# Kernel optimization log

Hardware: AMD Instinct MI355X
Metric: run time of the kernel (lower is better)

## Reference

```python
import jax, jax.numpy as jnp
from jax import lax
import numpy as np

KERNEL = 32
ORISIZE = 256
EPS = 1e-5


def _avgpool(x, k):
    # x: [B, C, H, W] -> [B, C, H-k+1, W-k+1], stride 1, VALID
    s = lax.reduce_window(x, 0.0, lax.add, (1, 1, k, k), (1, 1, 1, 1), 'VALID')
    return s / float(k * k)


def setup_inputs() -> dict:
    key = jax.random.key(0)
    k1, k2, k3, k4 = jax.random.split(key, 4)
    B, C = 32, 64
    return {
        'infeat': jax.random.normal(k1, (B, 2, ORISIZE, ORISIZE), jnp.float32),
        'labelTpesudo': jax.random.uniform(k2, (B, 1, ORISIZE, ORISIZE), jnp.float32),
        'labelT': jax.random.uniform(k3, (B, 1, ORISIZE, ORISIZE), jnp.float32),
        'FeatureDA': jax.random.normal(k4, (B, C, ORISIZE, ORISIZE), jnp.float32),
        'k': 2,
    }


def reference(infeat, labelTpesudo, labelT, FeatureDA, k):
    B = infeat.shape[0]
    P = ORISIZE - KERNEL + 1  # poolSize = 225
    half = KERNEL // 2        # suppression half-window = 16

    prob = jax.nn.softmax(infeat, axis=1)                      # F.softmax default dim=1 for 4D
    ent = -prob * jnp.log(prob + EPS)                          # Entropy()
    entP = jnp.sum(_avgpool(ent, KERNEL), axis=1)              # [B, P, P]
    featP = _avgpool(prob, KERNEL)                             # [B, 2, P, P]

    def extract(src, py, px):  # src [C,H,W] -> [C,KERNEL,KERNEL]
        return lax.dynamic_slice(src, (0, py, px), (src.shape[0], KERNEL, KERNEL))
    extract_b = jax.vmap(extract, in_axes=(0, 0, 0))

    grid = jnp.arange(P)
    cls_list, feat_list, lp_list, lt_list, val_list, oxy_list = [], [], [], [], [], []

    for c in range(2):  # class loop (unchg, chg)
        mask = jnp.ones((B, P, P), infeat.dtype)
        for _kk in range(k):  # greedy top-k with suppression
            filt = (featP[:, c] - 0.1 * entP) * mask           # [B, P, P]
            flat = filt.reshape(B, -1)
            idx = jnp.argmax(flat, axis=1)                     # topk k=1
            vals = jnp.take_along_axis(flat, idx[:, None], axis=1)[:, 0]
            py = idx // P
            px = idx % P
            # suppression box in pooled coords (half-open, clipped to [0, P])
            y0 = jnp.maximum(0, py - half); y1 = jnp.minimum(P, py + half)
            x0 = jnp.maximum(0, px - half); x1 = jnp.minimum(P, px + half)
            box = ((grid[None, :, None] >= y0[:, None, None]) & (grid[None, :, None] < y1[:, None, None]) &
                   (grid[None, None, :] >= x0[:, None, None]) & (grid[None, None, :] < x1[:, None, None]))
            mask = mask * (1.0 - box.astype(mask.dtype))
            # patch extraction in image coords: py,px <= P-1 so 32x32 always fits
            cls_list.append(extract_b(infeat, py, px))
            feat_list.append(extract_b(FeatureDA, py, px))
            lp_list.append(extract_b(labelTpesudo, py, px))
            lt_list.append(extract_b(labelT, py, px))
            val_list.append(vals)
            ox = jnp.stack([px, px + KERNEL - 1], axis=1)
            oy = jnp.stack([py, py + KERNEL - 1], axis=1)
            oxy_list.append(jnp.stack([ox, oy], axis=1).astype(jnp.int32))  # [B,2,2]

    classiferT = jnp.concatenate(cls_list, axis=0)   # [2*k*B, 2, 32, 32]
    patchFeatDA = jnp.concatenate(feat_list, axis=0)  # [2*k*B, C, 32, 32]
    labelpesudo = jnp.concatenate(lp_list, axis=0)
    labelTTrue = jnp.concatenate(lt_list, axis=0)
    provalue = jnp.concatenate(val_list, axis=0)      # [2*k*B]
    pointXY = jnp.concatenate(oxy_list, axis=0)       # [2*k*B, 2, 2]
    return classiferT, patchFeatDA, labelpesudo, labelTTrue, provalue, pointXY
```

## Files before the change

### kernel.cpp

```cpp
#include <hip/hip_runtime.h>
#include <math.h>

#define ORISIZE 256
#define KER 32
#define P 225
#define PP (P * P)
#define HALF 16
#define FEPS 1e-5f

__global__ __launch_bounds__(256) void field_hpool_kernel(
    const float* __restrict__ infeat, float* __restrict__ Hp,
    float* __restrict__ He) {
  int b = blockIdx.x >> 8;
  int y = blockIdx.x & 255;
  int x = threadIdx.x;

  __shared__ float sp[ORISIZE];
  __shared__ float se[ORISIZE];

  const float* r0 = infeat + ((size_t)(b * 2 + 0) * ORISIZE + y) * ORISIZE;
  const float* r1 = infeat + ((size_t)(b * 2 + 1) * ORISIZE + y) * ORISIZE;
  float a0 = r0[x];
  float a1 = r1[x];
  float m = fmaxf(a0, a1);
  float e0 = expf(a0 - m);
  float e1 = expf(a1 - m);
  float s = e0 + e1;
  float p0 = e0 / s;
  float p1 = e1 / s;
  float ent = -(p0 * logf(p0 + FEPS)) - (p1 * logf(p1 + FEPS));
  sp[x] = p0;
  se[x] = ent;
  __syncthreads();

  if (x < P) {
    float accp = 0.f, acce = 0.f;
#pragma unroll
    for (int dx = 0; dx < KER; ++dx) {
      accp += sp[x + dx];
      acce += se[x + dx];
    }
    size_t o = ((size_t)b * ORISIZE + y) * P + x;
    Hp[o] = accp;
    He[o] = acce;
  }
}

__global__ __launch_bounds__(256) void vpool_kernel(
    const float* __restrict__ Hp, const float* __restrict__ He,
    float* __restrict__ SP, float* __restrict__ EP, int total) {
  int idx = blockIdx.x * blockDim.x + threadIdx.x;
  if (idx >= total) return;
  int b = idx / PP;
  int r = idx - b * PP;
  int py = r / P;
  int px = r - py * P;
  const float* hp = Hp + ((size_t)b * ORISIZE + py) * P + px;
  const float* he = He + ((size_t)b * ORISIZE + py) * P + px;
  float a = 0.f, e = 0.f;
#pragma unroll
  for (int dy = 0; dy < KER; ++dy) {
    a += hp[(size_t)dy * P];
    e += he[(size_t)dy * P];
  }
  SP[idx] = a * (1.f / (KER * KER));
  EP[idx] = e * (1.f / (KER * KER));
}

__global__ __launch_bounds__(256) void select_kernel(
    const float* __restrict__ SP, const float* __restrict__ EP, int B, int K,
    float* __restrict__ out_val, float* __restrict__ out_xy,
    int* __restrict__ selyx) {
  int bc = blockIdx.x;
  int b = bc % B;
  int c = bc / B;
  int tid = threadIdx.x;

  __shared__ float rv[256];
  __shared__ int ri[256];
  __shared__ int bys[16], bxs[16];

  const float* sp = SP + (size_t)b * PP;
  const float* ep = EP + (size_t)b * PP;

  for (int kk = 0; kk < K; ++kk) {
    float best = -INFINITY;
    int bi = PP;
    for (int i = tid; i < PP; i += 256) {
      int py = i / P;
      int px = i - py * P;
      float sv = sp[i];
      float ev = ep[i];
      float v = ((c == 0) ? sv : 1.0f - sv) - 0.1f * ev;
      bool masked = false;
      for (int j = 0; j < kk; ++j) {
        if (py >= bys[j] - HALF && py < bys[j] + HALF && px >= bxs[j] - HALF &&
            px < bxs[j] + HALF)
          masked = true;
      }
      if (masked) v = 0.0f;
      if (v > best) {
        best = v;
        bi = i;
      }
    }
    rv[tid] = best;
    ri[tid] = bi;
    __syncthreads();
    for (int sh = 128; sh > 0; sh >>= 1) {
      if (tid < sh) {
        float v2 = rv[tid + sh];
        int i2 = ri[tid + sh];
        if (v2 > rv[tid] || (v2 == rv[tid] && i2 < ri[tid])) {
          rv[tid] = v2;
          ri[tid] = i2;
        }
      }
      __syncthreads();
    }
    if (tid == 0) {
      int idx = ri[0];
      int py = idx / P;
      int px = idx - py * P;
      bys[kk] = py;
      bxs[kk] = px;
      int slot = (c * K + kk) * B + b;
      out_val[slot] = rv[0];
      out_xy[slot * 4 + 0] = (float)px;
      out_xy[slot * 4 + 1] = (float)(px + KER - 1);
      out_xy[slot * 4 + 2] = (float)py;
      out_xy[slot * 4 + 3] = (float)(py + KER - 1);
      selyx[slot * 2 + 0] = py;
      selyx[slot * 2 + 1] = px;
    }
    __syncthreads();
  }
}

__global__ __launch_bounds__(256) void extract_kernel(
    const float* __restrict__ src, float* __restrict__ dst,
    const int* __restrict__ selyx, int Csrc, int B, int total) {
  int idx = blockIdx.x * blockDim.x + threadIdx.x;
  if (idx >= total) return;
  int per = Csrc * KER * KER;
  int slot = idx / per;
  int r = idx - slot * per;
  int ch = r / (KER * KER);
  int rr = r - ch * (KER * KER);
  int dy = rr >> 5;
  int dx = rr & 31;
  int b = slot % B;
  int py = selyx[slot * 2 + 0];
  int px = selyx[slot * 2 + 1];
  dst[idx] =
      src[(((size_t)b * Csrc + ch) * ORISIZE + (py + dy)) * ORISIZE + (px + dx)];
}

extern "C" void kernel_launch(void* const* d_in, const int* in_sizes, int n_in,
                              void* d_out, int out_size, void* d_ws,
                              size_t ws_size, hipStream_t stream) {
  const float* infeat = (const float*)d_in[0];
  const float* labelTpesudo = (const float*)d_in[1];
  const float* labelT = (const float*)d_in[2];
  const float* FeatureDA = (const float*)d_in[3];

  int B = in_sizes[0] / (2 * ORISIZE * ORISIZE);
  int C = in_sizes[3] / (B * ORISIZE * ORISIZE);
  long per_patch = (long)(C + 4) * KER * KER + 5;
  int K = (int)((long)out_size / (2L * B * per_patch));
  if (K < 1) K = 1;
  if (K > 16) K = 16;
  int npatch = 2 * K * B;

  float* Hp = (float*)d_ws;
  float* He = Hp + (size_t)B * ORISIZE * P;
  float* SP = He + (size_t)B * ORISIZE * P;
  float* EP = SP + (size_t)B * PP;
  int* selyx = (int*)(EP + (size_t)B * PP);

  float* out = (float*)d_out;
  size_t o_cls = 0;
  size_t o_feat = o_cls + (size_t)npatch * 2 * KER * KER;
  size_t o_lp = o_feat + (size_t)npatch * C * KER * KER;
  size_t o_lt = o_lp + (size_t)npatch * 1 * KER * KER;
  size_t o_val = o_lt + (size_t)npatch * 1 * KER * KER;
  size_t o_xy = o_val + (size_t)npatch;

  field_hpool_kernel<<<dim3(B * ORISIZE), dim3(256), 0, stream>>>(infeat, Hp,
                                                                  He);

  int totalv = B * PP;
  vpool_kernel<<<dim3((totalv + 255) / 256), dim3(256), 0, stream>>>(
      Hp, He, SP, EP, totalv);

  select_kernel<<<dim3(2 * B), dim3(256), 0, stream>>>(
      SP, EP, B, K, out + o_val, out + o_xy, selyx);

  int t_cls = npatch * 2 * KER * KER;
  extract_kernel<<<dim3((t_cls + 255) / 256), dim3(256), 0, stream>>>(
      infeat, out + o_cls, selyx, 2, B, t_cls);
  int t_feat = npatch * C * KER * KER;
  extract_kernel<<<dim3((t_feat + 255) / 256), dim3(256), 0, stream>>>(
      FeatureDA, out + o_feat, selyx, C, B, t_feat);
  int t_lab = npatch * 1 * KER * KER;
  extract_kernel<<<dim3((t_lab + 255) / 256), dim3(256), 0, stream>>>(
      labelTpesudo, out + o_lp, selyx, 1, B, t_lab);
  extract_kernel<<<dim3((t_lab + 255) / 256), dim3(256), 0, stream>>>(
      labelT, out + o_lt, selyx, 1, B, t_lab);
}
```

Before: 806.7 us.

## Split greedy argmax across many blocks per round and fuse patch extraction

The single-block-per-(batch,class) selection kernel, which ran only 64 blocks, is replaced by one launch per greedy round. Each launch spreads the pooled map over 32 blocks per (batch,class) and reduces the partial maxima in the next round or in a small finish kernel. The pooling kernel now writes the combined per-class score map directly, so selection no longer recomputes it. The four extraction launches are merged into one kernel. The cost is extra launches per round and a small re-reduction of the partial results in every block.

New measurement: 707.5 us. 12.3% less time.

```diff
diff --git a/kernel.cpp b/kernel.cpp
--- a/kernel.cpp
+++ b/kernel.cpp
@@ -7,6 +7,8 @@
 #define PP (P * P)
 #define HALF 16
 #define FEPS 1e-5f
+#define NSPLIT 32
+#define CHUNK ((PP + NSPLIT - 1) / NSPLIT)
 
 __global__ __launch_bounds__(256) void field_hpool_kernel(
     const float* __restrict__ infeat, float* __restrict__ Hp,
@@ -48,7 +50,7 @@
 
 __global__ __launch_bounds__(256) void vpool_kernel(
     const float* __restrict__ Hp, const float* __restrict__ He,
-    float* __restrict__ SP, float* __restrict__ EP, int total) {
+    float* __restrict__ F, int B, int total) {
   int idx = blockIdx.x * blockDim.x + threadIdx.x;
   if (idx >= total) return;
   int b = idx / PP;
@@ -63,97 +65,153 @@
     a += hp[(size_t)dy * P];
     e += he[(size_t)dy * P];
   }
-  SP[idx] = a * (1.f / (KER * KER));
-  EP[idx] = e * (1.f / (KER * KER));
-}
-
-__global__ __launch_bounds__(256) void select_kernel(
-    const float* __restrict__ SP, const float* __restrict__ EP, int B, int K,
+  float sv = a * (1.f / (KER * KER));
+  float ev = e * (1.f / (KER * KER));
+  F[(size_t)(0 * B + b) * PP + r] = sv - 0.1f * ev;
+  F[(size_t)(1 * B + b) * PP + r] = (1.0f - sv) - 0.1f * ev;
+}
+
+__global__ __launch_bounds__(256) void argmax_round_kernel(
+    const float* __restrict__ F, float* __restrict__ pval,
+    int* __restrict__ pidx, int B, int kk) {
+  int s = blockIdx.x;
+  int b = blockIdx.y;
+  int c = blockIdx.z;
+  int tid = threadIdx.x;
+
+  __shared__ int bys[16], bxs[16];
+  __shared__ float rv[256];
+  __shared__ int ri[256];
+
+  if (tid < kk) {
+    int j = tid;
+    int pbase = ((j * B + b) * 2 + c) * NSPLIT;
+    float bv = -INFINITY;
+    int bi = PP;
+    for (int ss = 0; ss < NSPLIT; ++ss) {
+      float v = pval[pbase + ss];
+      int ii = pidx[pbase + ss];
+      if (v > bv || (v == bv && ii < bi)) { bv = v; bi = ii; }
+    }
+    int py = bi / P;
+    bys[j] = py;
+    bxs[j] = bi - py * P;
+  }
+  __syncthreads();
+
+  const float* f = F + ((size_t)c * B + b) * PP;
+  int base = s * CHUNK;
+  int end = base + CHUNK;
+  if (end > PP) end = PP;
+
+  float best = -INFINITY;
+  int bi = PP;
+  for (int i = base + tid; i < end; i += 256) {
+    float v = f[i];
+    int py = i / P;
+    int px = i - py * P;
+    bool masked = false;
+    for (int j = 0; j < kk; ++j) {
+      if (py >= bys[j] - HALF && py < bys[j] + HALF && px >= bxs[j] - HALF &&
+          px < bxs[j] + HALF)
+        masked = true;
+    }
+    if (masked) v = 0.0f;
+    if (v > best) {
+      best = v;
+      bi = i;
+    }
+  }
+  rv[tid] = best;
+  ri[tid] = bi;
+  __syncthreads();
+  for (int sh = 128; sh > 0; sh >>= 1) {
+    if (tid < sh) {
+      float v2 = rv[tid + sh];
+      int i2 = ri[tid + sh];
+      if (v2 > rv[tid] || (v2 == rv[tid] && i2 < ri[tid])) {
+        rv[tid] = v2;
+        ri[tid] = i2;
+      }
+    }
+    __syncthreads();
+  }
+  if (tid == 0) {
+    int p = ((kk * B + b) * 2 + c) * NSPLIT + s;
+    pval[p] = rv[0];
+    pidx[p] = ri[0];
+  }
+}
+
+__global__ __launch_bounds__(256) void finish_kernel(
+    const float* __restrict__ pval, const int* __restrict__ pidx, int B, int K,
     float* __restrict__ out_val, float* __restrict__ out_xy,
     int* __restrict__ selyx) {
-  int bc = blockIdx.x;
-  int b = bc % B;
-  int c = bc / B;
-  int tid = threadIdx.x;
-
-  __shared__ float rv[256];
-  __shared__ int ri[256];
-  __shared__ int bys[16], bxs[16];
-
-  const float* sp = SP + (size_t)b * PP;
-  const float* ep = EP + (size_t)b * PP;
-
-  for (int kk = 0; kk < K; ++kk) {
-    float best = -INFINITY;
+  int total = B * 2 * K;
+  for (int t = blockIdx.x * blockDim.x + threadIdx.x; t < total;
+       t += gridDim.x * blockDim.x) {
+    int c = t & 1;
+    int rem = t >> 1;
+    int b = rem % B;
+    int kk = rem / B;
+    int pbase = ((kk * B + b) * 2 + c) * NSPLIT;
+    float bv = -INFINITY;
     int bi = PP;
-    for (int i = tid; i < PP; i += 256) {
-      int py = i / P;
-      int px = i - py * P;
-      float sv = sp[i];
-      float ev = ep[i];
-      float v = ((c == 0) ? sv : 1.0f - sv) - 0.1f * ev;
-      bool masked = false;
-      for (int j = 0; j < kk; ++j) {
-        if (py >= bys[j] - HALF && py < bys[j] + HALF && px >= bxs[j] - HALF &&
-            px < bxs[j] + HALF)
-          masked = true;
-      }
-      if (masked) v = 0.0f;
-      if (v > best) {
-        best = v;
-        bi = i;
-      }
-    }
-    rv[tid] = best;
-    ri[tid] = bi;
-    __syncthreads();
-    for (int sh = 128; sh > 0; sh >>= 1) {
-      if (tid < sh) {
-        float v2 = rv[tid + sh];
-        int i2 = ri[tid + sh];
-        if (v2 > rv[tid] || (v2 == rv[tid] && i2 < ri[tid])) {
-          rv[tid] = v2;
-          ri[tid] = i2;
-        }
-      }
-      __syncthreads();
-    }
-    if (tid == 0) {
-      int idx = ri[0];
-      int py = idx / P;
-      int px = idx - py * P;
-      bys[kk] = py;
-      bxs[kk] = px;
-      int slot = (c * K + kk) * B + b;
-      out_val[slot] = rv[0];
-      out_xy[slot * 4 + 0] = (float)px;
-      out_xy[slot * 4 + 1] = (float)(px + KER - 1);
-      out_xy[slot * 4 + 2] = (float)py;
-      out_xy[slot * 4 + 3] = (float)(py + KER - 1);
-      selyx[slot * 2 + 0] = py;
-      selyx[slot * 2 + 1] = px;
-    }
-    __syncthreads();
-  }
-}
-
-__global__ __launch_bounds__(256) void extract_kernel(
-    const float* __restrict__ src, float* __restrict__ dst,
-    const int* __restrict__ selyx, int Csrc, int B, int total) {
+    for (int ss = 0; ss < NSPLIT; ++ss) {
+      float v = pval[pbase + ss];
+      int ii = pidx[pbase + ss];
+      if (v > bv || (v == bv && ii < bi)) { bv = v; bi = ii; }
+    }
+    int py = bi / P;
+    int px = bi - py * P;
+    int slot = (c * K + kk) * B + b;
+    out_val[slot] = bv;
+    out_xy[slot * 4 + 0] = (float)px;
+    out_xy[slot * 4 + 1] = (float)(px + KER - 1);
+    out_xy[slot * 4 + 2] = (float)py;
+    out_xy[slot * 4 + 3] = (float)(py + KER - 1);
+    selyx[slot * 2 + 0] = py;
+    selyx[slot * 2 + 1] = px;
+  }
+}
+
+__global__ __launch_bounds__(256) void extract_all_kernel(
+    const float* __restrict__ infeat, const float* __restrict__ FeatureDA,
+    const float* __restrict__ lp, const float* __restrict__ lt,
+    const int* __restrict__ selyx, int B, int C, int total,
+    float* __restrict__ out, size_t o_feat, size_t o_lp, size_t o_lt) {
   int idx = blockIdx.x * blockDim.x + threadIdx.x;
   if (idx >= total) return;
-  int per = Csrc * KER * KER;
+  int TC = C + 4;
+  int per = TC * KER * KER;
   int slot = idx / per;
-  int r = idx - slot * per;
-  int ch = r / (KER * KER);
-  int rr = r - ch * (KER * KER);
-  int dy = rr >> 5;
-  int dx = rr & 31;
+  int rem = idx - slot * per;
+  int tc = rem >> 10;
+  int pix = rem & 1023;
+  int dy = pix >> 5;
+  int dx = pix & 31;
   int b = slot % B;
   int py = selyx[slot * 2 + 0];
   int px = selyx[slot * 2 + 1];
-  dst[idx] =
-      src[(((size_t)b * Csrc + ch) * ORISIZE + (py + dy)) * ORISIZE + (px + dx)];
+
+  const float* src;
+  int ch, srcC;
+  size_t dsto;
+  if (tc < 2) {
+    src = infeat; ch = tc; srcC = 2;
+    dsto = ((size_t)slot * 2 + ch) * 1024;
+  } else if (tc < 2 + C) {
+    src = FeatureDA; ch = tc - 2; srcC = C;
+    dsto = o_feat + ((size_t)slot * C + ch) * 1024;
+  } else if (tc == 2 + C) {
+    src = lp; ch = 0; srcC = 1;
+    dsto = o_lp + (size_t)slot * 1024;
+  } else {
+    src = lt; ch = 0; srcC = 1;
+    dsto = o_lt + (size_t)slot * 1024;
+  }
+  out[dsto + pix] =
+      src[(((size_t)b * srcC + ch) * ORISIZE + (py + dy)) * ORISIZE + (px + dx)];
 }
 
 extern "C" void kernel_launch(void* const* d_in, const int* in_sizes, int n_in,
@@ -174,16 +232,16 @@
 
   float* Hp = (float*)d_ws;
   float* He = Hp + (size_t)B * ORISIZE * P;
-  float* SP = He + (size_t)B * ORISIZE * P;
-  float* EP = SP + (size_t)B * PP;
-  int* selyx = (int*)(EP + (size_t)B * PP);
+  float* F = He + (size_t)B * ORISIZE * P;
+  float* pval = F + (size_t)2 * B * PP;
+  int* pidx = (int*)(pval + (size_t)16 * B * 2 * NSPLIT);
+  int* selyx = pidx + (size_t)16 * B * 2 * NSPLIT;
 
   float* out = (float*)d_out;
-  size_t o_cls = 0;
-  size_t o_feat = o_cls + (size_t)npatch * 2 * KER * KER;
+  size_t o_feat = (size_t)npatch * 2 * KER * KER;
   size_t o_lp = o_feat + (size_t)npatch * C * KER * KER;
-  size_t o_lt = o_lp + (size_t)npatch * 1 * KER * KER;
-  size_t o_val = o_lt + (size_t)npatch * 1 * KER * KER;
+  size_t o_lt = o_lp + (size_t)npatch * KER * KER;
+  size_t o_val = o_lt + (size_t)npatch * KER * KER;
   size_t o_xy = o_val + (size_t)npatch;
 
   field_hpool_kernel<<<dim3(B * ORISIZE), dim3(256), 0, stream>>>(infeat, Hp,
@@ -191,20 +249,18 @@
 
   int totalv = B * PP;
   vpool_kernel<<<dim3((totalv + 255) / 256), dim3(256), 0, stream>>>(
-      Hp, He, SP, EP, totalv);
-
-  select_kernel<<<dim3(2 * B), dim3(256), 0, stream>>>(
-      SP, EP, B, K, out + o_val, out + o_xy, selyx);
-
-  int t_cls = npatch * 2 * KER * KER;
-  extract_kernel<<<dim3((t_cls + 255) / 256), dim3(256), 0, stream>>>(
-      infeat, out + o_cls, selyx, 2, B, t_cls);
-  int t_feat = npatch * C * KER * KER;
-  extract_kernel<<<dim3((t_feat + 255) / 256), dim3(256), 0, stream>>>(
-      FeatureDA, out + o_feat, selyx, C, B, t_feat);
-  int t_lab = npatch * 1 * KER * KER;
-  extract_kernel<<<dim3((t_lab + 255) / 256), dim3(256), 0, stream>>>(
-      labelTpesudo, out + o_lp, selyx, 1, B, t_lab);
-  extract_kernel<<<dim3((t_lab + 255) / 256), dim3(256), 0, stream>>>(
-      labelT, out + o_lt, selyx, 1, B, t_lab);
-}
+      Hp, He, F, B, totalv);
+
+  for (int kk = 0; kk < K; ++kk) {
+    argmax_round_kernel<<<dim3(NSPLIT, B, 2), dim3(256), 0, stream>>>(
+        F, pval, pidx, B, kk);
+  }
+  finish_kernel<<<dim3(1), dim3(256), 0, stream>>>(pval, pidx, B, K,
+                                                   out + o_val, out + o_xy,
+                                                   selyx);
+
+  int total = npatch * (C + 4) * KER * KER;
+  extract_all_kernel<<<dim3((total + 255) / 256), dim3(256), 0, stream>>>(
+      infeat, FeatureDA, labelTpesudo, labelT, selyx, B, C, total, out, o_feat,
+      o_lp, o_lt);
+}
```
